# Kernel optimization log

Measured on AMD Instinct MI355X. Metric: run time of the kernel, lower is better.

## Reference

```python
import jax, jax.numpy as jnp
import numpy as np

VOCAB = 32000
HID = 1024
LAYERS = 6
HEADS = 8 * 2  # 16
HEAD_DIM = HID // HEADS
INTER = int(HID * 8 / 3)  # 2730, matches torch int(hidden*8/3)
MAX_POS = 2048
EPS = 1e-5


def setup_inputs() -> dict:
    key = jax.random.key(0)
    ks = jax.random.split(key, 16)
    B, S = 2, 1024
    input_ids = jax.random.randint(ks[0], (B, S), 0, VOCAB)

    def lin(k, out_d, in_d, stack=True):
        shape = (LAYERS, out_d, in_d) if stack else (out_d, in_d)
        return jax.random.normal(k, shape, jnp.float32) * (in_d ** -0.5)

    return {
        "input_ids": input_ids,
        "tok_emb": jax.random.normal(ks[1], (VOCAB, HID), jnp.float32) * 0.02,
        "pos_emb": jax.random.normal(ks[2], (MAX_POS, HID), jnp.float32) * 0.02,
        "qkv_w": lin(ks[3], 3 * HID, HID),
        "o_w": lin(ks[4], HID, HID),
        "gate_w": lin(ks[5], INTER, HID),
        "up_w": lin(ks[6], INTER, HID),
        "down_w": lin(ks[7], HID, INTER),
        "ln1_w": jnp.ones((LAYERS, HID), jnp.float32),
        "ln1_b": jnp.zeros((LAYERS, HID), jnp.float32),
        "ln2_w": jnp.ones((LAYERS, HID), jnp.float32),
        "ln2_b": jnp.zeros((LAYERS, HID), jnp.float32),
        "lnf_w": jnp.ones((HID,), jnp.float32),
        "lnf_b": jnp.zeros((HID,), jnp.float32),
        "head_w": lin(ks[8], VOCAB, HID, stack=False),
    }


def _layernorm(x, w, b):
    mu = jnp.mean(x, axis=-1, keepdims=True)
    var = jnp.mean(jnp.square(x - mu), axis=-1, keepdims=True)
    return (x - mu) * jax.lax.rsqrt(var + EPS) * w + b


def _forward(input_ids, tok_emb, pos_emb, qkv_w, o_w, gate_w, up_w, down_w,
             ln1_w, ln1_b, ln2_w, ln2_b, lnf_w, lnf_b, head_w):
    B, S = input_ids.shape
    h = tok_emb[input_ids] + pos_emb[jnp.arange(S)][None, :, :]  # [B,S,H]
    scale = HEAD_DIM ** -0.5

    def layer(h, p):
        qkv_w, o_w, gate_w, up_w, down_w, l1w, l1b, l2w, l2b = p
        # attention block
        x = _layernorm(h, l1w, l1b)
        qkv = jnp.einsum('bsh,oh->bso', x, qkv_w)  # [B,S,3H]
        qkv = qkv.reshape(B, S, 3, HEADS, HEAD_DIM)
        q, k, v = qkv[:, :, 0], qkv[:, :, 1], qkv[:, :, 2]  # [B,S,Hn,Dh]
        attn = jnp.einsum('bqnd,bknd->bnqk', q, k) * scale  # [B,Hn,S,S]
        attn = jax.nn.softmax(attn, axis=-1)
        ctx = jnp.einsum('bnqk,bknd->bqnd', attn, v).reshape(B, S, HID)
        h = h + jnp.einsum('bsh,oh->bso', ctx, o_w)
        # MLP block (SwiGLU)
        x = _layernorm(h, l2w, l2b)
        gate = jax.nn.silu(jnp.einsum('bsh,ih->bsi', x, gate_w))
        up = jnp.einsum('bsh,ih->bsi', x, up_w)
        h = h + jnp.einsum('bsi,hi->bsh', gate * up, down_w)
        return h, None

    h, _ = jax.lax.scan(layer, h, (qkv_w, o_w, gate_w, up_w, down_w,
                                   ln1_w, ln1_b, ln2_w, ln2_b))
    h = _layernorm(h, lnf_w, lnf_b)
    logits = jnp.einsum('bsh,vh->bsv', h, head_w)  # [B,S,V]
    return logits


def reference(input_ids, tok_emb, pos_emb, qkv_w, o_w, gate_w, up_w, down_w,
              ln1_w, ln1_b, ln2_w, ln2_b, lnf_w, lnf_b, head_w):
    return _forward(input_ids, tok_emb, pos_emb, qkv_w, o_w, gate_w, up_w,
                    down_w, ln1_w, ln1_b, ln2_w, ln2_b, lnf_w, lnf_b, head_w)
```

## Files before the change

kernel.cpp:

```cpp
#include <hip/hip_runtime.h>

typedef unsigned short u16;
typedef __attribute__((ext_vector_type(8))) short bf16x8;
typedef __attribute__((ext_vector_type(8))) unsigned short us8;
typedef __attribute__((ext_vector_type(4))) unsigned short us4;
typedef __attribute__((ext_vector_type(4))) float f32x4;

#define SEQ    1024
#define TOK    2048
#define HID    1024
#define NLAYER 6
#define NHEAD  16
#define HDIM   64
#define QKV3   3072
#define INTER  2730
#define IPAD   2816
#define VOCAB  32000
#define LN_EPS 1e-5f

__device__ __forceinline__ u16 f2bf(float f) {
  unsigned u = __float_as_uint(f);
  return (u16)((u + 0x7fffu + ((u >> 16) & 1u)) >> 16);
}
__device__ __forceinline__ float bf2f(u16 u) {
  return __uint_as_float(((unsigned)u) << 16);
}

__device__ __forceinline__ void gl_lds16(const void* g, void* l) {
  __builtin_amdgcn_global_load_lds(
      (const __attribute__((address_space(1))) void*)g,
      (__attribute__((address_space(3))) void*)l, 16, 0, 0);
}

__global__ __launch_bounds__(256) void embed_kernel(
    const int* __restrict__ ids, const float* __restrict__ tok,
    const float* __restrict__ pos, float* __restrict__ h)
{
  int t = blockIdx.x;
  int s = t & (SEQ - 1);
  int id = ids[t];
  int c = threadIdx.x * 4;
  float4 tv = *(const float4*)(tok + (long)id * HID + c);
  float4 pv = *(const float4*)(pos + (long)s * HID + c);
  float4 o;
  o.x = tv.x + pv.x; o.y = tv.y + pv.y; o.z = tv.z + pv.z; o.w = tv.w + pv.w;
  *(float4*)(h + (long)t * HID + c) = o;
}

__global__ __launch_bounds__(256) void ln_kernel(
    const float* __restrict__ h, const float* __restrict__ w,
    const float* __restrict__ b, u16* __restrict__ out)
{
  int t = blockIdx.x;
  int tid = threadIdx.x;
  int lane = tid & 63, wid = tid >> 6;
  float4 v = *(const float4*)(h + (long)t * HID + tid * 4);
  float s1 = v.x + v.y + v.z + v.w;
  float s2 = v.x * v.x + v.y * v.y + v.z * v.z + v.w * v.w;
#pragma unroll
  for (int o = 32; o > 0; o >>= 1) { s1 += __shfl_down(s1, o); s2 += __shfl_down(s2, o); }
  __shared__ float r1[4], r2[4];
  if (lane == 0) { r1[wid] = s1; r2[wid] = s2; }
  __syncthreads();
  float t1 = r1[0] + r1[1] + r1[2] + r1[3];
  float t2 = r2[0] + r2[1] + r2[2] + r2[3];
  float mu = t1 * (1.f / HID);
  float var = t2 * (1.f / HID) - mu * mu;
  float rs = rsqrtf(var + LN_EPS);
  float4 wv = *(const float4*)(w + tid * 4);
  float4 bv = *(const float4*)(b + tid * 4);
  us4 o4;
  o4[0] = f2bf((v.x - mu) * rs * wv.x + bv.x);
  o4[1] = f2bf((v.y - mu) * rs * wv.y + bv.y);
  o4[2] = f2bf((v.z - mu) * rs * wv.z + bv.z);
  o4[3] = f2bf((v.w - mu) * rs * wv.w + bv.w);
  *(us4*)(out + (long)t * HID + tid * 4) = o4;
}

__global__ __launch_bounds__(256) void cvt_kernel(
    const float* __restrict__ src, u16* __restrict__ dst,
    int N, int K, int Kpad, long total8)
{
  long i = (long)blockIdx.x * 256 + threadIdx.x;
  if (i >= total8) return;
  int kp8 = Kpad >> 3;
  int n = (int)(i / kp8);
  int kc = (int)(i % kp8);
  us8 o;
#pragma unroll
  for (int j = 0; j < 8; ++j) {
    int k = kc * 8 + j;
    float v = (n < N && k < K) ? src[(long)n * K + k] : 0.f;
    o[j] = f2bf(v);
  }
  *(us8*)(dst + i * 8) = o;
}

__global__ __launch_bounds__(256) void cvt_layer_kernel(
    const float* __restrict__ qkv_w, const float* __restrict__ o_w,
    const float* __restrict__ gate, const float* __restrict__ up,
    const float* __restrict__ down,
    u16* __restrict__ wq, u16* __restrict__ wo,
    u16* __restrict__ wgu, u16* __restrict__ wd)
{
  long i = (long)blockIdx.x * 256 + threadIdx.x;
  us8 o;
  if (i < 393216L) {
    const float* s = qkv_w + i * 8;
#pragma unroll
    for (int j = 0; j < 8; ++j) o[j] = f2bf(s[j]);
    *(us8*)(wq + i * 8) = o;
  } else if (i < 524288L) {
    long i2 = i - 393216L;
    const float* s = o_w + i2 * 8;
#pragma unroll
    for (int j = 0; j < 8; ++j) o[j] = f2bf(s[j]);
    *(us8*)(wo + i2 * 8) = o;
  } else if (i < 1245184L) {
    long i3 = i - 524288L;
    int n = (int)(i3 >> 7);
    int kc = (int)(i3 & 127);
    int g = n >> 1;
    const float* s = (n & 1) ? up : gate;
#pragma unroll
    for (int j = 0; j < 8; ++j) {
      int k = kc * 8 + j;
      o[j] = f2bf((g < INTER) ? s[(long)g * HID + k] : 0.f);
    }
    *(us8*)(wgu + i3 * 8) = o;
  } else {
    long i4 = i - 1245184L;
    int n = (int)(i4 / 352);
    int kc = (int)(i4 % 352);
#pragma unroll
    for (int j = 0; j < 8; ++j) {
      int k = kc * 8 + j;
      o[j] = f2bf((k < INTER) ? down[(long)n * INTER + k] : 0.f);
    }
    *(us8*)(wd + i4 * 8) = o;
  }
}

__global__ __launch_bounds__(256) void vtrans_kernel(
    const u16* __restrict__ qkv, u16* __restrict__ vT)
{
  int gid = blockIdx.x * 256 + threadIdx.x;
  int d  = gid & 63;
  int kc = (gid >> 6) & 127;
  int z  = gid >> 13;
  int b = z >> 4, hh = z & 15;
  const u16* src = qkv + (long)b * SEQ * QKV3 + 2048 + hh * 64 + d;
  us8 v;
#pragma unroll
  for (int j = 0; j < 8; ++j) v[j] = src[(long)(kc * 8 + j) * QKV3];
  *(us8*)(vT + (long)z * 65536 + (long)d * 1024 + kc * 8) = v;
}

__global__ __launch_bounds__(256, 3) void attn_kernel(
    const u16* __restrict__ qkv, const u16* __restrict__ vT,
    u16* __restrict__ ctx)
{
  __shared__ u16 Ks[8][128][8];
  __shared__ u16 Vs[16][64][8];
  __shared__ u16 Ps[4][16 * 128];

  const int tid  = threadIdx.x;
  const int lane = tid & 63;
  const int w    = tid >> 6;
  const int lo   = lane & 15;
  const int hi   = lane >> 4;

  const int z  = blockIdx.x & 31;
  const int qt = blockIdx.x >> 5;
  const int b  = z >> 4, h = z & 15;

  const u16* Qb  = qkv + (long)b * SEQ * QKV3 + h * 64;
  const u16* Kb  = Qb + 1024;
  const u16* Vtb = vT + (long)z * 65536;

  bf16x8 q[2];
#pragma unroll
  for (int ks = 0; ks < 2; ++ks)
    q[ks] = *(const bf16x8*)(Qb + (long)(qt * 64 + w * 16 + lo) * QKV3 + ks * 32 + hi * 8);

  f32x4 po[4];
  float m_run[4], l_run[4];
#pragma unroll
  for (int r = 0; r < 4; ++r) { m_run[r] = -1e30f; l_run[r] = 0.f; }
#pragma unroll
  for (int nd = 0; nd < 4; ++nd) po[nd] = (f32x4){0.f, 0.f, 0.f, 0.f};

  char* Pw = (char*)&Ps[w][0];

  for (int c = 0; c < 8; ++c) {
#pragma unroll
    for (int i = 0; i < 4; ++i) {
      int u = w * 4 + i, g = u & 7, rg = u >> 3;
      gl_lds16(Kb + (long)(c * 128 + rg * 64 + lane) * QKV3 + g * 8, &Ks[g][rg * 64][0]);
    }
#pragma unroll
    for (int i = 0; i < 4; ++i) {
      int kg = w * 4 + i;
      gl_lds16(Vtb + (long)lane * 1024 + c * 128 + kg * 8, &Vs[kg][0][0]);
    }
    __syncthreads();

    f32x4 s[8];
#pragma unroll
    for (int jf = 0; jf < 8; ++jf) s[jf] = (f32x4){0.f, 0.f, 0.f, 0.f};
#pragma unroll
    for (int jf = 0; jf < 8; ++jf) {
      bf16x8 bk[2];
#pragma unroll
      for (int ks = 0; ks < 2; ++ks)
        bk[ks] = *(const bf16x8*)&Ks[ks * 4 + hi][jf * 16 + lo][0];
#pragma unroll
      for (int ks = 0; ks < 2; ++ks)
        s[jf] = __builtin_amdgcn_mfma_f32_16x16x32_bf16(q[ks], bk[ks], s[jf], 0, 0, 0);
    }

    float scf[4];
#pragma unroll
    for (int r = 0; r < 4; ++r) {
      float rm = -1e30f;
#pragma unroll
      for (int jf = 0; jf < 8; ++jf) {
        s[jf][r] *= 0.125f;
        rm = fmaxf(rm, s[jf][r]);
      }
#pragma unroll
      for (int o = 1; o < 16; o <<= 1) rm = fmaxf(rm, __shfl_xor(rm, o));
      float mn = fmaxf(m_run[r], rm);
      float sc = __expf(m_run[r] - mn);
      float rs = 0.f;
#pragma unroll
      for (int jf = 0; jf < 8; ++jf) {
        float e = __expf(s[jf][r] - mn);
        s[jf][r] = e;
        rs += e;
      }
#pragma unroll
      for (int o = 1; o < 16; o <<= 1) rs += __shfl_xor(rs, o);
      l_run[r] = l_run[r] * sc + rs;
      m_run[r] = mn;
      scf[r] = sc;
    }

#pragma unroll
    for (int jf = 0; jf < 8; ++jf)
#pragma unroll
      for (int r = 0; r < 4; ++r) {
        int row = hi * 4 + r;
        int byo = row * 256 + ((((jf * 16 + lo) * 2)) ^ ((row & 7) << 4));
        *(u16*)(Pw + byo) = f2bf(s[jf][r]);
      }
#pragma unroll
    for (int nd = 0; nd < 4; ++nd)
#pragma unroll
      for (int r = 0; r < 4; ++r) po[nd][r] *= scf[r];

    bf16x8 pa[4];
#pragma unroll
    for (int ks2 = 0; ks2 < 4; ++ks2) {
      int row = lo;
      int byo = row * 256 + (((ks2 * 32 + hi * 8) * 2) ^ ((row & 7) << 4));
      pa[ks2] = *(const bf16x8*)(Pw + byo);
    }
#pragma unroll
    for (int nd = 0; nd < 4; ++nd) {
      bf16x8 bv[4];
#pragma unroll
      for (int ks2 = 0; ks2 < 4; ++ks2)
        bv[ks2] = *(const bf16x8*)&Vs[ks2 * 4 + hi][nd * 16 + lo][0];
#pragma unroll
      for (int ks2 = 0; ks2 < 4; ++ks2)
        po[nd] = __builtin_amdgcn_mfma_f32_16x16x32_bf16(pa[ks2], bv[ks2], po[nd], 0, 0, 0);
    }
    __syncthreads();
  }

#pragma unroll
  for (int r = 0; r < 4; ++r) {
    float inv = 1.f / l_run[r];
    int qrow = qt * 64 + w * 16 + hi * 4 + r;
    u16* dst = ctx + (long)(b * SEQ + qrow) * HID + h * 64;
#pragma unroll
    for (int nd = 0; nd < 4; ++nd)
      dst[nd * 16 + lo] = f2bf(po[nd][r] * inv);
  }
}

template<int BM, int BN, int EPI>
__global__ __launch_bounds__(256) void gemm_bt(
    const u16* __restrict__ A, const u16* __restrict__ B,
    void* __restrict__ Cv, const float* __restrict__ resid,
    int lda, int ldb, int ldc, int K, float scale, int bdiv,
    long sA1, long sA2, long sB1, long sB2, long sC1, long sC2)
{
  constexpr int FM = BM / 32;
  constexpr int FN = BN / 32;
  __shared__ u16 As[2][BM * 32];
  __shared__ u16 Bs[2][BN * 32];

  const int tid = threadIdx.x;
  const int lane = tid & 63;
  const int wid = tid >> 6;
  const int wm = wid >> 1, wn = wid & 1;

  const int z = blockIdx.z;
  const long offA = (long)(z / bdiv) * sA1 + (long)(z % bdiv) * sA2;
  const long offB = (long)(z / bdiv) * sB1 + (long)(z % bdiv) * sB2;
  const long offC = (long)(z / bdiv) * sC1 + (long)(z % bdiv) * sC2;

  const u16* Ab = A + offA + (long)blockIdx.x * BM * lda;
  const u16* Bb = B + offB + (long)blockIdx.y * BN * ldb;

  auto stage = [&](int buf, int kt) {
    const u16* a = Ab + (long)kt * 32;
    const u16* bsrc = Bb + (long)kt * 32;
#pragma unroll
    for (int i = 0; i < BM / 64; ++i) {
      int row = i * 64 + wid * 16 + (lane >> 2);
      gl_lds16(a + (long)row * lda + (lane & 3) * 8, &As[buf][i * 2048 + wid * 512]);
    }
#pragma unroll
    for (int i = 0; i < BN / 64; ++i) {
      int row = i * 64 + wid * 16 + (lane >> 2);
      gl_lds16(bsrc + (long)row * ldb + (lane & 3) * 8, &Bs[buf][i * 2048 + wid * 512]);
    }
  };

  f32x4 acc[FM][FN];
#pragma unroll
  for (int i = 0; i < FM; ++i)
#pragma unroll
    for (int j = 0; j < FN; ++j) acc[i][j] = (f32x4){0.f, 0.f, 0.f, 0.f};

  int aoff[FM], boff[FN];
#pragma unroll
  for (int i = 0; i < FM; ++i)
    aoff[i] = (wm * (BM / 2) + i * 16 + (lane & 15)) * 32 + (lane >> 4) * 8;
#pragma unroll
  for (int j = 0; j < FN; ++j)
    boff[j] = (wn * (BN / 2) + j * 16 + (lane & 15)) * 32 + (lane >> 4) * 8;

  const int KT = K >> 5;
  stage(0, 0);
  __syncthreads();
  int cur = 0;
  for (int kt = 0; kt < KT; ++kt) {
    if (kt + 1 < KT) stage(cur ^ 1, kt + 1);
    bf16x8 av[FM], bv[FN];
#pragma unroll
    for (int i = 0; i < FM; ++i) av[i] = *(const bf16x8*)&As[cur][aoff[i]];
#pragma unroll
    for (int j = 0; j < FN; ++j) bv[j] = *(const bf16x8*)&Bs[cur][boff[j]];
#pragma unroll
    for (int i = 0; i < FM; ++i)
#pragma unroll
      for (int j = 0; j < FN; ++j)
        acc[i][j] = __builtin_amdgcn_mfma_f32_16x16x32_bf16(av[i], bv[j], acc[i][j], 0, 0, 0);
    __syncthreads();
    cur ^= 1;
  }

  const int r0 = blockIdx.x * BM + wm * (BM / 2) + (lane >> 4) * 4;
  const int c0 = blockIdx.y * BN + wn * (BN / 2) + (lane & 15);
#pragma unroll
  for (int i = 0; i < FM; ++i) {
#pragma unroll
    for (int j = 0; j < FN; ++j) {
      f32x4 v = acc[i][j];
#pragma unroll
      for (int r = 0; r < 4; ++r) {
        if (EPI == 3) {
          float pv = __shfl_xor(v[r], 1);
          if ((lane & 1) == 0) {
            float gf = v[r];
            float res = gf / (1.f + __expf(-gf)) * pv;
            int cc = c0 + j * 16;
            long idx = offC + (long)(r0 + i * 16 + r) * ldc + (cc >> 1);
            ((u16*)Cv)[idx] = f2bf(res);
          }
        } else {
          long idx = offC + (long)(r0 + i * 16 + r) * ldc + (c0 + j * 16);
          if (EPI == 0)       ((u16*)Cv)[idx] = f2bf(v[r] * scale);
          else if (EPI == 1)  ((float*)Cv)[idx] = v[r] * scale;
          else                ((float*)Cv)[idx] = resid[idx] + v[r];
        }
      }
    }
  }
}

template<int EPI>
__global__ __launch_bounds__(512, 1) void gemm256(
    const u16* __restrict__ A, const u16* __restrict__ B,
    void* __restrict__ Cv, int NB, int ldc)
{
  __shared__ u16 lds[2][2][2][8][128][8];

  const int tid  = threadIdx.x;
  const int lane = tid & 63;
  const int w    = tid >> 6;
  const int wm   = w >> 2;
  const int wn   = w & 3;
  const int arow = lane & 15;
  const int kg   = lane >> 4;

  const int flat = blockIdx.x;
  const int swz  = (flat & 7) * NB + (flat >> 3);
  const int bm   = swz & 7;
  const int bn   = swz >> 3;

  const u16* Ab = A + (long)bm * 256 * 1024;
  const u16* Bb = B + (long)bn * 256 * 1024;

  auto stage = [&](int mat, int d, int half, int t) {
#pragma unroll
    for (int i = 0; i < 2; ++i) {
      const int u  = w * 2 + i;
      const int g  = u & 7;
      const int rg = u >> 3;
      const u16* src = (mat == 0 ? Ab : Bb)
                     + (long)(half * 128 + rg * 64 + lane) * 1024 + t * 64 + g * 8;
      gl_lds16(src, &lds[d][mat][half][g][rg * 64][0]);
    }
  };

  f32x4 acc[2][2][4][2];
#pragma unroll
  for (int qm = 0; qm < 2; ++qm)
#pragma unroll
    for (int qn = 0; qn < 2; ++qn)
#pragma unroll
      for (int f = 0; f < 4; ++f)
#pragma unroll
        for (int n = 0; n < 2; ++n) acc[qm][qn][f][n] = (f32x4){0.f, 0.f, 0.f, 0.f};

  bf16x8 a[4][2];
  bf16x8 b[2][2][2];

  auto rdA = [&](int d, int qm) {
#pragma unroll
    for (int f = 0; f < 4; ++f)
#pragma unroll
      for (int ks = 0; ks < 2; ++ks)
        a[f][ks] = *(const bf16x8*)&lds[d][0][wm][ks * 4 + kg][qm * 64 + f * 16 + arow][0];
  };
  auto rdB = [&](int d, int qn) {
#pragma unroll
    for (int n = 0; n < 2; ++n)
#pragma unroll
      for (int ks = 0; ks < 2; ++ks)
        b[qn][n][ks] = *(const bf16x8*)&lds[d][1][wn >> 1][ks * 4 + kg]
                                          [(wn & 1) * 64 + qn * 32 + n * 16 + arow][0];
  };
  auto mm = [&](int qm, int qn) {
#pragma unroll
    for (int f = 0; f < 4; ++f)
#pragma unroll
      for (int n = 0; n < 2; ++n)
#pragma unroll
        for (int ks = 0; ks < 2; ++ks)
          acc[qm][qn][f][n] = __builtin_amdgcn_mfma_f32_16x16x32_bf16(
              a[f][ks], b[qn][n][ks], acc[qm][qn][f][n], 0, 0, 0);
  };

#define BAR asm volatile("s_barrier" ::: "memory")
#define PRIO1 __builtin_amdgcn_s_setprio(1)
#define PRIO0 __builtin_amdgcn_s_setprio(0)

  stage(1, 0, 0, 0);
  stage(0, 0, 0, 0);
  stage(0, 0, 1, 0);
  stage(1, 0, 1, 0);
  stage(1, 1, 0, 1);
  stage(0, 1, 0, 1);
  asm volatile("s_waitcnt vmcnt(4)" ::: "memory");
  BAR;

  const int iters = 8;
#pragma unroll 1
  for (int it = 0; it < iters; ++it) {
    const int T = 2 * it;
    const bool pf = (it + 1 < iters);
    rdA(0, 0); rdB(0, 0); rdB(0, 1);
    stage(0, 1, 1, T + 1);
    stage(1, 1, 1, T + 1);
    BAR; PRIO1; mm(0, 0); mm(0, 1); PRIO0; BAR;
    rdA(0, 1);
    if (pf) { stage(1, 0, 0, T + 2);
              stage(0, 0, 0, T + 2); }
    BAR; PRIO1; mm(1, 0); mm(1, 1); PRIO0;
    if (pf) asm volatile("s_waitcnt vmcnt(4)" ::: "memory");
    else    asm volatile("s_waitcnt vmcnt(0)" ::: "memory");
    BAR;
    rdA(1, 0); rdB(1, 0); rdB(1, 1);
    if (pf) { stage(0, 0, 1, T + 2);
              stage(1, 0, 1, T + 2); }
    BAR; PRIO1; mm(0, 0); mm(0, 1); PRIO0; BAR;
    rdA(1, 1);
    if (pf) { stage(1, 1, 0, T + 3);
              stage(0, 1, 0, T + 3); }
    BAR; PRIO1; mm(1, 0); mm(1, 1); PRIO0;
    if (pf) asm volatile("s_waitcnt vmcnt(4)" ::: "memory");
    BAR;
  }
#undef BAR
#undef PRIO1
#undef PRIO0

#pragma unroll
  for (int qm = 0; qm < 2; ++qm) {
#pragma unroll
    for (int qn = 0; qn < 2; ++qn) {
#pragma unroll
      for (int f = 0; f < 4; ++f) {
        const int r0 = bm * 256 + wm * 128 + qm * 64 + f * 16 + kg * 4;
#pragma unroll
        for (int n = 0; n < 2; ++n) {
          const int c = bn * 256 + wn * 64 + qn * 32 + n * 16 + arow;
          f32x4 v = acc[qm][qn][f][n];
#pragma unroll
          for (int r = 0; r < 4; ++r) {
            long idx = (long)(r0 + r) * ldc + c;
            if (EPI == 0) ((u16*)Cv)[idx] = f2bf(v[r]);
            else          ((float*)Cv)[idx] = v[r];
          }
        }
      }
    }
  }
}

extern "C" void kernel_launch(void* const* d_in, const int* in_sizes, int n_in,
                              void* d_out, int out_size, void* d_ws, size_t ws_size,
                              hipStream_t stream)
{
  (void)in_sizes; (void)n_in; (void)out_size; (void)ws_size;
  const int*   ids     = (const int*)d_in[0];
  const float* tok_emb = (const float*)d_in[1];
  const float* pos_emb = (const float*)d_in[2];
  const float* qkv_w   = (const float*)d_in[3];
  const float* o_w     = (const float*)d_in[4];
  const float* gate_w  = (const float*)d_in[5];
  const float* up_w    = (const float*)d_in[6];
  const float* down_w  = (const float*)d_in[7];
  const float* ln1_w   = (const float*)d_in[8];
  const float* ln1_b   = (const float*)d_in[9];
  const float* ln2_w   = (const float*)d_in[10];
  const float* ln2_b   = (const float*)d_in[11];
  const float* lnf_w   = (const float*)d_in[12];
  const float* lnf_b   = (const float*)d_in[13];
  const float* head_w  = (const float*)d_in[14];

  char* ws = (char*)d_ws;
  long off = 0;
  auto alloc = [&](long bytes) { void* p = ws + off; off += (bytes + 1023) & ~1023L; return p; };
  float* h   = (float*)alloc((long)TOK * HID * 4);
  u16*   x   = (u16*)  alloc((long)TOK * HID * 2);
  u16*   qkv = (u16*)  alloc((long)TOK * QKV3 * 2);
  u16*   vT  = (u16*)  alloc(32L * HDIM * SEQ * 2);
  u16*   ctx = (u16*)  alloc((long)TOK * HID * 2);
  u16*   y   = (u16*)  alloc((long)TOK * IPAD * 2);
  u16*   whead = (u16*)alloc((long)VOCAB * HID * 2);
  u16* wq  = whead;
  u16* wo  = wq + 3072 * 1024;
  u16* wgu = wo + 1024 * 1024;
  u16* wd  = wgu + 5632 * 1024;

  embed_kernel<<<TOK, 256, 0, stream>>>(ids, tok_emb, pos_emb, h);

  for (int l = 0; l < NLAYER; ++l) {
    cvt_layer_kernel<<<6272, 256, 0, stream>>>(
        qkv_w + (long)l * QKV3 * HID, o_w + (long)l * HID * HID,
        gate_w + (long)l * INTER * HID, up_w + (long)l * INTER * HID,
        down_w + (long)l * HID * INTER, wq, wo, wgu, wd);

    ln_kernel<<<TOK, 256, 0, stream>>>(h, ln1_w + l * HID, ln1_b + l * HID, x);

    gemm_bt<128, 128, 0><<<dim3(16, 24, 1), 256, 0, stream>>>(
        x, wq, qkv, nullptr, HID, HID, QKV3, HID, 1.f, 1, 0, 0, 0, 0, 0, 0);

    vtrans_kernel<<<1024, 256, 0, stream>>>(qkv, vT);

    attn_kernel<<<dim3(512), 256, 0, stream>>>(qkv, vT, ctx);

    gemm_bt<64, 128, 2><<<dim3(32, 8, 1), 256, 0, stream>>>(
        ctx, wo, h, h, HID, HID, HID, HID, 1.f, 1, 0, 0, 0, 0, 0, 0);

    ln_kernel<<<TOK, 256, 0, stream>>>(h, ln2_w + l * HID, ln2_b + l * HID, x);

    gemm_bt<128, 128, 3><<<dim3(16, 44, 1), 256, 0, stream>>>(
        x, wgu, y, nullptr, HID, HID, IPAD, HID, 1.f, 1, 0, 0, 0, 0, 0, 0);

    gemm_bt<64, 128, 2><<<dim3(32, 8, 1), 256, 0, stream>>>(
        y, wd, h, h, IPAD, IPAD, HID, IPAD, 1.f, 1, 0, 0, 0, 0, 0, 0);
  }

  ln_kernel<<<TOK, 256, 0, stream>>>(h, lnf_w, lnf_b, x);
  cvt_kernel<<<16000, 256, 0, stream>>>(head_w, whead, VOCAB, HID, HID, 4096000L);
  gemm256<1><<<dim3(1000), 512, 0, stream>>>(x, whead, d_out, 125, VOCAB);
}
```

Measured before the change: 1.378 ms.

## Fuse LN with weight conversion and V-transpose into QKV GEMM epilogue

Measured after the change: 1.236 ms. 10.3% less time.

```diff
diff --git a/kernel.cpp b/kernel.cpp
--- a/kernel.cpp
+++ b/kernel.cpp
@@ -47,19 +47,16 @@
   *(float4*)(h + (long)t * HID + c) = o;
 }
 
-__global__ __launch_bounds__(256) void ln_kernel(
-    const float* __restrict__ h, const float* __restrict__ w,
-    const float* __restrict__ b, u16* __restrict__ out)
-{
-  int t = blockIdx.x;
-  int tid = threadIdx.x;
+__device__ __forceinline__ void ln_body(
+    int t, int tid, const float* __restrict__ h, const float* __restrict__ w,
+    const float* __restrict__ b, u16* __restrict__ out, float* r1, float* r2)
+{
   int lane = tid & 63, wid = tid >> 6;
   float4 v = *(const float4*)(h + (long)t * HID + tid * 4);
   float s1 = v.x + v.y + v.z + v.w;
   float s2 = v.x * v.x + v.y * v.y + v.z * v.z + v.w * v.w;
 #pragma unroll
   for (int o = 32; o > 0; o >>= 1) { s1 += __shfl_down(s1, o); s2 += __shfl_down(s2, o); }
-  __shared__ float r1[4], r2[4];
   if (lane == 0) { r1[wid] = s1; r2[wid] = s2; }
   __syncthreads();
   float t1 = r1[0] + r1[1] + r1[2] + r1[3];
@@ -77,33 +74,30 @@
   *(us4*)(out + (long)t * HID + tid * 4) = o4;
 }
 
-__global__ __launch_bounds__(256) void cvt_kernel(
-    const float* __restrict__ src, u16* __restrict__ dst,
-    int N, int K, int Kpad, long total8)
-{
-  long i = (long)blockIdx.x * 256 + threadIdx.x;
-  if (i >= total8) return;
-  int kp8 = Kpad >> 3;
-  int n = (int)(i / kp8);
-  int kc = (int)(i % kp8);
-  us8 o;
-#pragma unroll
-  for (int j = 0; j < 8; ++j) {
-    int k = kc * 8 + j;
-    float v = (n < N && k < K) ? src[(long)n * K + k] : 0.f;
-    o[j] = f2bf(v);
-  }
-  *(us8*)(dst + i * 8) = o;
-}
-
-__global__ __launch_bounds__(256) void cvt_layer_kernel(
+__global__ __launch_bounds__(256) void ln_kernel(
+    const float* __restrict__ h, const float* __restrict__ w,
+    const float* __restrict__ b, u16* __restrict__ out)
+{
+  __shared__ float r1[4], r2[4];
+  ln_body(blockIdx.x, threadIdx.x, h, w, b, out, r1, r2);
+}
+
+__global__ __launch_bounds__(256) void pre_kernel(
+    const float* __restrict__ h, const float* __restrict__ lw,
+    const float* __restrict__ lb, u16* __restrict__ x,
     const float* __restrict__ qkv_w, const float* __restrict__ o_w,
     const float* __restrict__ gate, const float* __restrict__ up,
     const float* __restrict__ down,
     u16* __restrict__ wq, u16* __restrict__ wo,
     u16* __restrict__ wgu, u16* __restrict__ wd)
 {
-  long i = (long)blockIdx.x * 256 + threadIdx.x;
+  __shared__ float r1[4], r2[4];
+  int bid = blockIdx.x;
+  if (bid < 2048) {
+    ln_body(bid, threadIdx.x, h, lw, lb, x, r1, r2);
+    return;
+  }
+  long i = (long)(bid - 2048) * 256 + threadIdx.x;
   us8 o;
   if (i < 393216L) {
     const float* s = qkv_w + i * 8;
@@ -141,19 +135,23 @@
   }
 }
 
-__global__ __launch_bounds__(256) void vtrans_kernel(
-    const u16* __restrict__ qkv, u16* __restrict__ vT)
-{
-  int gid = blockIdx.x * 256 + threadIdx.x;
-  int d  = gid & 63;
-  int kc = (gid >> 6) & 127;
-  int z  = gid >> 13;
-  int b = z >> 4, hh = z & 15;
-  const u16* src = qkv + (long)b * SEQ * QKV3 + 2048 + hh * 64 + d;
-  us8 v;
-#pragma unroll
-  for (int j = 0; j < 8; ++j) v[j] = src[(long)(kc * 8 + j) * QKV3];
-  *(us8*)(vT + (long)z * 65536 + (long)d * 1024 + kc * 8) = v;
+__global__ __launch_bounds__(256) void fin_kernel(
+    const float* __restrict__ h, const float* __restrict__ lw,
+    const float* __restrict__ lb, u16* __restrict__ x,
+    const float* __restrict__ head_w, u16* __restrict__ whead)
+{
+  __shared__ float r1[4], r2[4];
+  int bid = blockIdx.x;
+  if (bid < 2048) {
+    ln_body(bid, threadIdx.x, h, lw, lb, x, r1, r2);
+    return;
+  }
+  long i = (long)(bid - 2048) * 256 + threadIdx.x;
+  const float* s = head_w + i * 8;
+  us8 o;
+#pragma unroll
+  for (int j = 0; j < 8; ++j) o[j] = f2bf(s[j]);
+  *(us8*)(whead + i * 8) = o;
 }
 
 __global__ __launch_bounds__(256, 3) void attn_kernel(
@@ -299,8 +297,12 @@
 {
   constexpr int FM = BM / 32;
   constexpr int FN = BN / 32;
-  __shared__ u16 As[2][BM * 32];
-  __shared__ u16 Bs[2][BN * 32];
+  constexpr int TRW = 136;
+  constexpr int SMEMU = (EPI == 4 && 128 * TRW > 2 * (BM + BN) * 32)
+                        ? 128 * TRW : 2 * (BM + BN) * 32;
+  __shared__ u16 smem[SMEMU];
+  auto absb = [&](int buf) { return smem + buf * (BM * 32); };
+  auto bsb  = [&](int buf) { return smem + 2 * (BM * 32) + buf * (BN * 32); };
 
   const int tid = threadIdx.x;
   const int lane = tid & 63;
@@ -321,12 +323,12 @@
 #pragma unroll
     for (int i = 0; i < BM / 64; ++i) {
       int row = i * 64 + wid * 16 + (lane >> 2);
-      gl_lds16(a + (long)row * lda + (lane & 3) * 8, &As[buf][i * 2048 + wid * 512]);
+      gl_lds16(a + (long)row * lda + (lane & 3) * 8, absb(buf) + i * 2048 + wid * 512);
     }
 #pragma unroll
     for (int i = 0; i < BN / 64; ++i) {
       int row = i * 64 + wid * 16 + (lane >> 2);
-      gl_lds16(bsrc + (long)row * ldb + (lane & 3) * 8, &Bs[buf][i * 2048 + wid * 512]);
+      gl_lds16(bsrc + (long)row * ldb + (lane & 3) * 8, bsb(buf) + i * 2048 + wid * 512);
     }
   };
 
@@ -352,9 +354,9 @@
     if (kt + 1 < KT) stage(cur ^ 1, kt + 1);
     bf16x8 av[FM], bv[FN];
 #pragma unroll
-    for (int i = 0; i < FM; ++i) av[i] = *(const bf16x8*)&As[cur][aoff[i]];
-#pragma unroll
-    for (int j = 0; j < FN; ++j) bv[j] = *(const bf16x8*)&Bs[cur][boff[j]];
+    for (int i = 0; i < FM; ++i) av[i] = *(const bf16x8*)(absb(cur) + aoff[i]);
+#pragma unroll
+    for (int j = 0; j < FN; ++j) bv[j] = *(const bf16x8*)(bsb(cur) + boff[j]);
 #pragma unroll
     for (int i = 0; i < FM; ++i)
 #pragma unroll
@@ -366,6 +368,37 @@
 
   const int r0 = blockIdx.x * BM + wm * (BM / 2) + (lane >> 4) * 4;
   const int c0 = blockIdx.y * BN + wn * (BN / 2) + (lane & 15);
+
+  if (EPI == 4 && blockIdx.y >= 16) {
+    u16* Tr = smem;
+    const int clb = wn * 64 + (lane & 15);
+    const int rlb = wm * 64 + (lane >> 4) * 4;
+#pragma unroll
+    for (int i = 0; i < FM; ++i) {
+#pragma unroll
+      for (int j = 0; j < FN; ++j) {
+        us4 t4;
+#pragma unroll
+        for (int r = 0; r < 4; ++r) t4[r] = f2bf(acc[i][j][r]);
+        *(us4*)(Tr + (clb + j * 16) * TRW + rlb + i * 16) = t4;
+      }
+    }
+    __syncthreads();
+    const int bb  = blockIdx.x >> 3;
+    const int k0  = (blockIdx.x & 7) * 128;
+    const int vcb = blockIdx.y * 128 - 2048;
+    const int c_loc = tid >> 1, half = tid & 1;
+    const int vcol = vcb + c_loc;
+    u16* vTo = (u16*)(void*)resid;
+    u16* dst = vTo + (long)(bb * 16 + (vcol >> 6)) * 65536
+             + (long)(vcol & 63) * 1024 + k0 + half * 64;
+    const u16* srcl = Tr + c_loc * TRW + half * 64;
+#pragma unroll
+    for (int j = 0; j < 8; ++j)
+      *(us8*)(dst + j * 8) = *(const us8*)(srcl + j * 8);
+    return;
+  }
+
 #pragma unroll
   for (int i = 0; i < FM; ++i) {
 #pragma unroll
@@ -384,9 +417,9 @@
           }
         } else {
           long idx = offC + (long)(r0 + i * 16 + r) * ldc + (c0 + j * 16);
-          if (EPI == 0)       ((u16*)Cv)[idx] = f2bf(v[r] * scale);
-          else if (EPI == 1)  ((float*)Cv)[idx] = v[r] * scale;
-          else                ((float*)Cv)[idx] = resid[idx] + v[r];
+          if (EPI == 0 || EPI == 4) ((u16*)Cv)[idx] = f2bf(v[r] * scale);
+          else if (EPI == 1)        ((float*)Cv)[idx] = v[r] * scale;
+          else                      ((float*)Cv)[idx] = resid[idx] + v[r];
         }
       }
     }
@@ -573,17 +606,14 @@
   embed_kernel<<<TOK, 256, 0, stream>>>(ids, tok_emb, pos_emb, h);
 
   for (int l = 0; l < NLAYER; ++l) {
-    cvt_layer_kernel<<<6272, 256, 0, stream>>>(
+    pre_kernel<<<8320, 256, 0, stream>>>(
+        h, ln1_w + l * HID, ln1_b + l * HID, x,
         qkv_w + (long)l * QKV3 * HID, o_w + (long)l * HID * HID,
         gate_w + (long)l * INTER * HID, up_w + (long)l * INTER * HID,
         down_w + (long)l * HID * INTER, wq, wo, wgu, wd);
 
-    ln_kernel<<<TOK, 256, 0, stream>>>(h, ln1_w + l * HID, ln1_b + l * HID, x);
-
-    gemm_bt<128, 128, 0><<<dim3(16, 24, 1), 256, 0, stream>>>(
-        x, wq, qkv, nullptr, HID, HID, QKV3, HID, 1.f, 1, 0, 0, 0, 0, 0, 0);
-
-    vtrans_kernel<<<1024, 256, 0, stream>>>(qkv, vT);
+    gemm_bt<128, 128, 4><<<dim3(16, 24, 1), 256, 0, stream>>>(
+        x, wq, qkv, (const float*)vT, HID, HID, QKV3, HID, 1.f, 1, 0, 0, 0, 0, 0, 0);
 
     attn_kernel<<<dim3(512), 256, 0, stream>>>(qkv, vT, ctx);
 
@@ -599,7 +629,6 @@
         y, wd, h, h, IPAD, IPAD, HID, IPAD, 1.f, 1, 0, 0, 0, 0, 0, 0);
   }
 
-  ln_kernel<<<TOK, 256, 0, stream>>>(h, lnf_w, lnf_b, x);
-  cvt_kernel<<<16000, 256, 0, stream>>>(head_w, whead, VOCAB, HID, HID, 4096000L);
+  fin_kernel<<<18048, 256, 0, stream>>>(h, lnf_w, lnf_b, x, head_w, whead);
   gemm256<1><<<dim3(1000), 512, 0, stream>>>(x, whead, d_out, 125, VOCAB);
 }
```
